# Optimization experiments

Measured on AMD Instinct MI355X. Metric: run time of the kernel, lower is better.

## Reference

```python
import jax, jax.numpy as jnp
import numpy as np

N_NODES = 50000
N_EDGES = 1600000
IN_FEATS = 128
HID = 128
HEADS = 4
F_HEAD = HID // HEADS  # 32
NEG_SLOPE = 0.2


def setup_inputs() -> dict:
    key = jax.random.key(0)
    ks = jax.random.split(key, 7)
    feat = jax.random.normal(ks[0], (N_NODES, IN_FEATS), dtype=jnp.float32)
    # Xavier-ish scaling for the shared fc weight
    W = jax.random.normal(ks[1], (IN_FEATS, HID), dtype=jnp.float32) * (1.0 / np.sqrt(IN_FEATS))
    attn_l = jax.random.normal(ks[2], (HEADS, F_HEAD), dtype=jnp.float32) * 0.1
    attn_r = jax.random.normal(ks[3], (HEADS, F_HEAD), dtype=jnp.float32) * 0.1
    bias = jnp.zeros((HID,), dtype=jnp.float32)
    src_idx = jax.random.randint(ks[4], (N_EDGES,), 0, N_NODES, dtype=jnp.int32)
    dst_idx = jax.random.randint(ks[5], (N_EDGES,), 0, N_NODES, dtype=jnp.int32)
    return {"feat": feat, "W": W, "attn_l": attn_l, "attn_r": attn_r,
            "bias": bias, "src_idx": src_idx, "dst_idx": dst_idx}


def reference(feat, W, attn_l, attn_r, bias, src_idx, dst_idx):
    N = feat.shape[0]
    # shared linear projection, split into heads: [N, H, F]
    ft = (feat @ W).reshape(N, HEADS, F_HEAD)
    # per-node attention logits: [N, H]
    el = jnp.einsum('nhf,hf->nh', ft, attn_l)
    er = jnp.einsum('nhf,hf->nh', ft, attn_r)
    # per-edge unnormalized score: [E, H]
    e = jax.nn.leaky_relu(el[src_idx] + er[dst_idx], negative_slope=NEG_SLOPE)
    # numerically stable edge softmax grouped by destination node
    m = jax.ops.segment_max(e, dst_idx, num_segments=N)          # [N, H]
    m = jnp.where(jnp.isfinite(m), m, 0.0)                       # guard empty dst
    a = jnp.exp(e - m[dst_idx])                                  # [E, H]
    s = jax.ops.segment_sum(a, dst_idx, num_segments=N)          # [N, H]
    alpha = a / jnp.where(s[dst_idx] > 0, s[dst_idx], 1.0)       # [E, H]
    # weighted scatter-sum aggregation: [N, H, F]
    msgs = ft[src_idx] * alpha[:, :, None]
    out = jax.ops.segment_sum(msgs, dst_idx, num_segments=N)
    out = out + bias.reshape(1, HEADS, F_HEAD)
    return out.reshape(N, HEADS * F_HEAD)  # flatten(1)
```

## Files before the change

### kernel.cpp

```cpp
#include <hip/hip_runtime.h>
#include <hip/hip_bf16.h>
#include <math.h>

#define NEG_SLOPE 0.2f
#define NBMAX 1024
#define CAP_E 2560
#define CH 4096

typedef __attribute__((ext_vector_type(8))) short short8;
typedef __attribute__((ext_vector_type(4))) float f32x4;
union BU { uint4 u; short8 s; };

__device__ __forceinline__ unsigned bf16rne(float f) {
    unsigned u = __float_as_uint(f);
    return (u + 0x7fffu + ((u >> 16) & 1u)) >> 16;
}
__device__ __forceinline__ short bf16s(float f) { return (short)bf16rne(f); }

__global__ __launch_bounds__(1024) void k_prepscat(
    const float* __restrict__ W, const float* __restrict__ attn_l,
    const float* __restrict__ attn_r, uint4* __restrict__ Wfrag,
    float4* __restrict__ WL, float4* __restrict__ WR,
    const int* __restrict__ src, const int* __restrict__ dst,
    int* __restrict__ gcur, unsigned* __restrict__ B, int E, int NB) {
    if (blockIdx.x < 3) {
        int gtid = blockIdx.x * 1024 + threadIdx.x;
        if (gtid < 2048) {
            int lane = gtid & 63;
            int ki = (gtid >> 6) & 3;
            int t = (gtid >> 8) & 3;
            int cg = gtid >> 10;
            int col = cg * 64 + t * 16 + (lane & 15);
            int kb = ki * 32 + (lane >> 4) * 8;
            unsigned d[4];
#pragma unroll
            for (int p = 0; p < 4; ++p) {
                unsigned lo = bf16rne(W[(kb + 2 * p) * 128 + col]);
                unsigned hi = bf16rne(W[(kb + 2 * p + 1) * 128 + col]);
                d[p] = lo | (hi << 16);
            }
            Wfrag[gtid] = make_uint4(d[0], d[1], d[2], d[3]);
        } else if (gtid < 2048 + 128) {
            int k = gtid - 2048;
            const float* wr_ = W + k * 128;
            float l0 = 0, l1 = 0, l2 = 0, l3 = 0, r0 = 0, r1 = 0, r2 = 0, r3 = 0;
            for (int j = 0; j < 32; ++j) {
                l0 += wr_[j] * attn_l[j];
                l1 += wr_[32 + j] * attn_l[32 + j];
                l2 += wr_[64 + j] * attn_l[64 + j];
                l3 += wr_[96 + j] * attn_l[96 + j];
                r0 += wr_[j] * attn_r[j];
                r1 += wr_[32 + j] * attn_r[32 + j];
                r2 += wr_[64 + j] * attn_r[64 + j];
                r3 += wr_[96 + j] * attn_r[96 + j];
            }
            WL[k] = make_float4(l0, l1, l2, l3);
            WR[k] = make_float4(r0, r1, r2, r3);
        }
        return;
    }
    __shared__ int h[NBMAX];
    __shared__ int lc[NBMAX];
    __shared__ int dl[CH];
    int tid = threadIdx.x;
    for (int t = tid; t < NB; t += 1024) h[t] = 0;
    __syncthreads();
    int beg = (blockIdx.x - 3) * CH;
    int end = min(beg + CH, E);
    for (int i = beg + tid; i < end; i += 1024) {
        int d = dst[i];
        dl[i - beg] = d;
        atomicAdd(&h[d >> 6], 1);
    }
    __syncthreads();
    for (int t = tid; t < NB; t += 1024)
        lc[t] = (h[t] > 0) ? atomicAdd(&gcur[t], h[t]) : 0;
    __syncthreads();
    for (int i = beg + tid; i < end; i += 1024) {
        int d = dl[i - beg];
        int pos = atomicAdd(&lc[d >> 6], 1);
        if (pos < CAP_E)
            B[(size_t)(d >> 6) * CAP_E + pos] = ((unsigned)src[i] << 6) | (unsigned)(d & 63);
    }
}

__global__ __launch_bounds__(512) void k_fcsort(
    const unsigned* __restrict__ B, const int* __restrict__ gcur,
    unsigned short* __restrict__ srt16, uint2* __restrict__ od,
    const float* __restrict__ feat, const uint4* __restrict__ Wfrag,
    const f32x4* __restrict__ WL, const f32x4* __restrict__ WR,
    unsigned* __restrict__ ftbf, float* __restrict__ el, float* __restrict__ er,
    int N, int NB) {
    __shared__ f32x4 WLs[128], WRs[128];
    __shared__ int hist[64];
    __shared__ int cur[64];
    const int tid = threadIdx.x;

    if (blockIdx.x < NB) {
        const int b = blockIdx.x;
        const int m = min(gcur[b], CAP_E);
        const size_t base = (size_t)b * CAP_E;
        if (tid < 64) hist[tid] = 0;
        __syncthreads();
        for (int i = tid; i < m; i += 512) atomicAdd(&hist[B[base + i] & 63], 1);
        __syncthreads();
        int v0 = (tid < 64) ? hist[tid] : 0;
        for (int off = 1; off < 64; off <<= 1) {
            int t = (tid < 64 && tid >= off) ? hist[tid - off] : 0;
            __syncthreads();
            if (tid < 64) hist[tid] += t;
            __syncthreads();
        }
        if (tid < 64) {
            int ex = hist[tid] - v0;
            cur[tid] = ex;
            int node = (b << 6) + tid;
            if (node < N) od[node] = make_uint2((unsigned)(base + ex), (unsigned)v0);
        }
        __syncthreads();
        for (int i = tid; i < m; i += 512) {
            unsigned p = B[base + i];
            int pos = atomicAdd(&cur[p & 63], 1);
            srt16[base + pos] = (unsigned short)(p >> 6);
        }
        return;
    }

    const int fb = blockIdx.x - NB;
    if (tid < 128) WLs[tid] = WL[tid];
    else if (tid < 256) WRs[tid - 128] = WR[tid - 128];
    __syncthreads();
    const int sub = tid >> 8;
    const int t256 = tid & 255;
    const int wave4 = t256 >> 6;
    const int lane = tid & 63;
    const int rt = wave4 & 1, cg = wave4 >> 1;
    const int nbase = fb * 64 + sub * 32 + rt * 16;
    const int row = nbase + (lane & 15);
    const int rowc = min(row, N - 1);
    const int q = lane >> 4;

    BU b[4][4];
#pragma unroll
    for (int t = 0; t < 4; ++t)
#pragma unroll
        for (int ki = 0; ki < 4; ++ki)
            b[t][ki].u = Wfrag[cg * 1024 + t * 256 + ki * 64 + lane];

    f32x4 acc0 = {0, 0, 0, 0}, acc1 = {0, 0, 0, 0}, acc2 = {0, 0, 0, 0}, acc3 = {0, 0, 0, 0};
    f32x4 elacc = {0, 0, 0, 0}, eracc = {0, 0, 0, 0};
    const float* fr = feat + (size_t)rowc * 128;
#pragma unroll
    for (int ki = 0; ki < 4; ++ki) {
        float4 f0 = *(const float4*)(fr + ki * 32 + q * 8);
        float4 f1 = *(const float4*)(fr + ki * 32 + q * 8 + 4);
        short8 a;
        a[0] = bf16s(f0.x); a[1] = bf16s(f0.y); a[2] = bf16s(f0.z); a[3] = bf16s(f0.w);
        a[4] = bf16s(f1.x); a[5] = bf16s(f1.y); a[6] = bf16s(f1.z); a[7] = bf16s(f1.w);
        acc0 = __builtin_amdgcn_mfma_f32_16x16x32_bf16(a, b[0][ki].s, acc0, 0, 0, 0);
        acc1 = __builtin_amdgcn_mfma_f32_16x16x32_bf16(a, b[1][ki].s, acc1, 0, 0, 0);
        acc2 = __builtin_amdgcn_mfma_f32_16x16x32_bf16(a, b[2][ki].s, acc2, 0, 0, 0);
        acc3 = __builtin_amdgcn_mfma_f32_16x16x32_bf16(a, b[3][ki].s, acc3, 0, 0, 0);
        if (cg == 0) {
            int kb = ki * 32 + q * 8;
            elacc += f0.x * WLs[kb + 0]; eracc += f0.x * WRs[kb + 0];
            elacc += f0.y * WLs[kb + 1]; eracc += f0.y * WRs[kb + 1];
            elacc += f0.z * WLs[kb + 2]; eracc += f0.z * WRs[kb + 2];
            elacc += f0.w * WLs[kb + 3]; eracc += f0.w * WRs[kb + 3];
            elacc += f1.x * WLs[kb + 4]; eracc += f1.x * WRs[kb + 4];
            elacc += f1.y * WLs[kb + 5]; eracc += f1.y * WRs[kb + 5];
            elacc += f1.z * WLs[kb + 6]; eracc += f1.z * WRs[kb + 6];
            elacc += f1.w * WLs[kb + 7]; eracc += f1.w * WRs[kb + 7];
        }
    }
#pragma unroll
    for (int t = 0; t < 4; ++t) {
#pragma unroll
        for (int r = 0; r < 4; ++r) {
            float d = (t == 0) ? acc0[r] : (t == 1) ? acc1[r] : (t == 2) ? acc2[r] : acc3[r];
            unsigned m = bf16rne(d);
            unsigned nb = (unsigned)__shfl_xor((int)m, 1, 64);
            int node = nbase + q * 4 + r;
            if (!(lane & 1) && node < N)
                ftbf[(size_t)node * 64 + cg * 32 + t * 8 + ((lane & 15) >> 1)] = m | (nb << 16);
        }
    }
    if (cg == 0) {
#pragma unroll
        for (int c = 0; c < 4; ++c) {
            elacc[c] += __shfl_xor(elacc[c], 16, 64);
            eracc[c] += __shfl_xor(eracc[c], 16, 64);
            elacc[c] += __shfl_xor(elacc[c], 32, 64);
            eracc[c] += __shfl_xor(eracc[c], 32, 64);
        }
        if (lane < 16 && row < N) {
            *(float4*)(el + (size_t)row * 4) = make_float4(elacc[0], elacc[1], elacc[2], elacc[3]);
            *(float4*)(er + (size_t)row * 4) = make_float4(eracc[0], eracc[1], eracc[2], eracc[3]);
        }
    }
}

__global__ __launch_bounds__(256) void k_aggregate(
    const unsigned* __restrict__ ftbf, const float* __restrict__ el,
    const float* __restrict__ er, const unsigned short* __restrict__ srt16,
    const uint2* __restrict__ od, const float* __restrict__ bias,
    float* __restrict__ out, int N) {
    __shared__ float als[4][64][4];
    __shared__ int snl[4][64];
    const int wave = threadIdx.x >> 6;
    const int lane = threadIdx.x & 63;
    const int l15 = lane & 15;
    const int hd = l15 >> 2;
    const int g = lane >> 4;
    int node = blockIdx.x * 4 + wave;
    if (node >= N) return;
    uint2 o = od[node];
    int beg = (int)o.x, cnt = (int)o.y;
    float4 erd = *(const float4*)(er + (size_t)node * 4);
    const uint4* ftv = (const uint4*)ftbf;

    float s0 = 0.f, s1 = 0.f, s2 = 0.f, s3 = 0.f;
    float ac0 = 0, ac1 = 0, ac2 = 0, ac3 = 0, ac4 = 0, ac5 = 0, ac6 = 0, ac7 = 0;
    for (int tile = 0; tile < cnt; tile += 64) {
        int tc = min(64, cnt - tile);
        float a0 = 0.f, a1 = 0.f, a2 = 0.f, a3 = 0.f;
        int sn = 0;
        if (lane < tc) {
            sn = srt16[beg + tile + lane];
            float4 a = *(const float4*)(el + (size_t)sn * 4);
            float e0 = a.x + erd.x; e0 = fmaxf(e0, NEG_SLOPE * e0);
            float e1 = a.y + erd.y; e1 = fmaxf(e1, NEG_SLOPE * e1);
            float e2 = a.z + erd.z; e2 = fmaxf(e2, NEG_SLOPE * e2);
            float e3 = a.w + erd.w; e3 = fmaxf(e3, NEG_SLOPE * e3);
            a0 = __expf(e0); a1 = __expf(e1);
            a2 = __expf(e2); a3 = __expf(e3);
        }
        s0 += a0; s1 += a1; s2 += a2; s3 += a3;
        *(float4*)(&als[wave][lane][0]) = make_float4(a0, a1, a2, a3);
        snl[wave][lane] = sn;
#pragma unroll 2
        for (int jj0 = 0; jj0 < tc; jj0 += 4) {
            int jj = jj0 + g;
            int j2 = (jj < tc) ? jj : (tc - 1);
            float af = als[wave][j2][hd];
            if (jj >= tc) af = 0.f;
            int s = snl[wave][j2];
            uint4 u = ftv[((size_t)s << 4) + l15];
            ac0 = fmaf(__uint_as_float(u.x << 16), af, ac0);
            ac1 = fmaf(__uint_as_float(u.x & 0xffff0000u), af, ac1);
            ac2 = fmaf(__uint_as_float(u.y << 16), af, ac2);
            ac3 = fmaf(__uint_as_float(u.y & 0xffff0000u), af, ac3);
            ac4 = fmaf(__uint_as_float(u.z << 16), af, ac4);
            ac5 = fmaf(__uint_as_float(u.z & 0xffff0000u), af, ac5);
            ac6 = fmaf(__uint_as_float(u.w << 16), af, ac6);
            ac7 = fmaf(__uint_as_float(u.w & 0xffff0000u), af, ac7);
        }
    }
#pragma unroll
    for (int off = 16; off <= 32; off <<= 1) {
        ac0 += __shfl_xor(ac0, off, 64);
        ac1 += __shfl_xor(ac1, off, 64);
        ac2 += __shfl_xor(ac2, off, 64);
        ac3 += __shfl_xor(ac3, off, 64);
        ac4 += __shfl_xor(ac4, off, 64);
        ac5 += __shfl_xor(ac5, off, 64);
        ac6 += __shfl_xor(ac6, off, 64);
        ac7 += __shfl_xor(ac7, off, 64);
    }
#pragma unroll
    for (int off = 32; off >= 1; off >>= 1) {
        s0 += __shfl_xor(s0, off, 64);
        s1 += __shfl_xor(s1, off, 64);
        s2 += __shfl_xor(s2, off, 64);
        s3 += __shfl_xor(s3, off, 64);
    }
    float ssel = (hd == 0) ? s0 : (hd == 1) ? s1 : (hd == 2) ? s2 : s3;
    float inv = ssel > 0.f ? 1.f / ssel : 0.f;
    if (lane < 16) {
        int c0 = lane * 8;
        float4 b0 = *(const float4*)(bias + c0);
        float4 b1 = *(const float4*)(bias + c0 + 4);
        float4 o0, o1;
        o0.x = ac0 * inv + b0.x; o0.y = ac1 * inv + b0.y;
        o0.z = ac2 * inv + b0.z; o0.w = ac3 * inv + b0.w;
        o1.x = ac4 * inv + b1.x; o1.y = ac5 * inv + b1.y;
        o1.z = ac6 * inv + b1.z; o1.w = ac7 * inv + b1.w;
        *(float4*)(out + (size_t)node * 128 + c0) = o0;
        *(float4*)(out + (size_t)node * 128 + c0 + 4) = o1;
    }
}

extern "C" void kernel_launch(void* const* d_in, const int* in_sizes, int n_in,
                              void* d_out, int out_size, void* d_ws, size_t ws_size,
                              hipStream_t stream) {
    const float* feat = (const float*)d_in[0];
    const float* W = (const float*)d_in[1];
    const float* attn_l = (const float*)d_in[2];
    const float* attn_r = (const float*)d_in[3];
    const float* bias = (const float*)d_in[4];
    const int* src = (const int*)d_in[5];
    const int* dst = (const int*)d_in[6];
    const int N = in_sizes[0] / 128;
    const int E = in_sizes[5];
    const int NB = (N + 63) >> 6;
    float* out = (float*)d_out;

    char* p = (char*)d_ws;
    unsigned int* ftbf = (unsigned int*)p;      p += (size_t)N * 64 * 4;
    unsigned* B = (unsigned*)p;                 p += ((size_t)NB * CAP_E * 4 + 15) & ~15ull;
    unsigned short* srt16 = (unsigned short*)p; p += ((size_t)NB * CAP_E * 2 + 15) & ~15ull;
    float* el = (float*)p;                      p += (size_t)N * 4 * 4;
    float* er = (float*)p;                      p += (size_t)N * 4 * 4;
    uint2* od = (uint2*)p;                      p += (size_t)N * 8;
    int* gcur = (int*)p;                        p += ((size_t)NB * 4 + 15) & ~15ull;
    uint4* Wfrag = (uint4*)p;                   p += 2048 * 16;
    float4* WL = (float4*)p;                    p += 128 * 16;
    float4* WR = (float4*)p;                    p += 128 * 16;

    int eblocks = (E + CH - 1) / CH;
    int fcblocks = (N + 63) / 64;
    hipMemsetAsync(gcur, 0, (size_t)NB * 4, stream);
    k_prepscat<<<3 + eblocks, 1024, 0, stream>>>(W, attn_l, attn_r, Wfrag, WL, WR,
                                                 src, dst, gcur, B, E, NB);
    k_fcsort<<<NB + fcblocks, 512, 0, stream>>>(B, gcur, srt16, od, feat, Wfrag,
                                                (const f32x4*)WL, (const f32x4*)WR,
                                                ftbf, el, er, N, NB);
    k_aggregate<<<(N + 3) / 4, 256, 0, stream>>>(ftbf, el, er, srt16, od, bias, out, N);
}
```

Baseline: 111.9 us.

## Regroup kernels so edge scatter overlaps node projection, split sort out

```diff
diff --git a/kernel.cpp b/kernel.cpp
--- a/kernel.cpp
+++ b/kernel.cpp
@@ -5,7 +5,7 @@
 #define NEG_SLOPE 0.2f
 #define NBMAX 1024
 #define CAP_E 2560
-#define CH 4096
+#define CH 8192
 
 typedef __attribute__((ext_vector_type(8))) short short8;
 typedef __attribute__((ext_vector_type(4))) float f32x4;
@@ -17,116 +17,84 @@
 }
 __device__ __forceinline__ short bf16s(float f) { return (short)bf16rne(f); }
 
-__global__ __launch_bounds__(1024) void k_prepscat(
+__global__ __launch_bounds__(1024) void k_prep0(
     const float* __restrict__ W, const float* __restrict__ attn_l,
     const float* __restrict__ attn_r, uint4* __restrict__ Wfrag,
     float4* __restrict__ WL, float4* __restrict__ WR,
+    int* __restrict__ gcur, int NB) {
+    int gtid = blockIdx.x * 1024 + threadIdx.x;
+    if (gtid < 2048) {
+        int lane = gtid & 63;
+        int ki = (gtid >> 6) & 3;
+        int t = (gtid >> 8) & 3;
+        int cg = gtid >> 10;
+        int col = cg * 64 + t * 16 + (lane & 15);
+        int kb = ki * 32 + (lane >> 4) * 8;
+        unsigned d[4];
+#pragma unroll
+        for (int p = 0; p < 4; ++p) {
+            unsigned lo = bf16rne(W[(kb + 2 * p) * 128 + col]);
+            unsigned hi = bf16rne(W[(kb + 2 * p + 1) * 128 + col]);
+            d[p] = lo | (hi << 16);
+        }
+        Wfrag[gtid] = make_uint4(d[0], d[1], d[2], d[3]);
+    } else if (gtid < 2048 + 128) {
+        int k = gtid - 2048;
+        const float* wr_ = W + k * 128;
+        float l0 = 0, l1 = 0, l2 = 0, l3 = 0, r0 = 0, r1 = 0, r2 = 0, r3 = 0;
+        for (int j = 0; j < 32; ++j) {
+            l0 += wr_[j] * attn_l[j];
+            l1 += wr_[32 + j] * attn_l[32 + j];
+            l2 += wr_[64 + j] * attn_l[64 + j];
+            l3 += wr_[96 + j] * attn_l[96 + j];
+            r0 += wr_[j] * attn_r[j];
+            r1 += wr_[32 + j] * attn_r[32 + j];
+            r2 += wr_[64 + j] * attn_r[64 + j];
+            r3 += wr_[96 + j] * attn_r[96 + j];
+        }
+        WL[k] = make_float4(l0, l1, l2, l3);
+        WR[k] = make_float4(r0, r1, r2, r3);
+    } else if (gtid - 2176 < NB) {
+        gcur[gtid - 2176] = 0;
+    }
+}
+
+__global__ __launch_bounds__(512) void k_megascat(
     const int* __restrict__ src, const int* __restrict__ dst,
-    int* __restrict__ gcur, unsigned* __restrict__ B, int E, int NB) {
-    if (blockIdx.x < 3) {
-        int gtid = blockIdx.x * 1024 + threadIdx.x;
-        if (gtid < 2048) {
-            int lane = gtid & 63;
-            int ki = (gtid >> 6) & 3;
-            int t = (gtid >> 8) & 3;
-            int cg = gtid >> 10;
-            int col = cg * 64 + t * 16 + (lane & 15);
-            int kb = ki * 32 + (lane >> 4) * 8;
-            unsigned d[4];
-#pragma unroll
-            for (int p = 0; p < 4; ++p) {
-                unsigned lo = bf16rne(W[(kb + 2 * p) * 128 + col]);
-                unsigned hi = bf16rne(W[(kb + 2 * p + 1) * 128 + col]);
-                d[p] = lo | (hi << 16);
-            }
-            Wfrag[gtid] = make_uint4(d[0], d[1], d[2], d[3]);
-        } else if (gtid < 2048 + 128) {
-            int k = gtid - 2048;
-            const float* wr_ = W + k * 128;
-            float l0 = 0, l1 = 0, l2 = 0, l3 = 0, r0 = 0, r1 = 0, r2 = 0, r3 = 0;
-            for (int j = 0; j < 32; ++j) {
-                l0 += wr_[j] * attn_l[j];
-                l1 += wr_[32 + j] * attn_l[32 + j];
-                l2 += wr_[64 + j] * attn_l[64 + j];
-                l3 += wr_[96 + j] * attn_l[96 + j];
-                r0 += wr_[j] * attn_r[j];
-                r1 += wr_[32 + j] * attn_r[32 + j];
-                r2 += wr_[64 + j] * attn_r[64 + j];
-                r3 += wr_[96 + j] * attn_r[96 + j];
-            }
-            WL[k] = make_float4(l0, l1, l2, l3);
-            WR[k] = make_float4(r0, r1, r2, r3);
-        }
-        return;
-    }
-    __shared__ int h[NBMAX];
-    __shared__ int lc[NBMAX];
-    __shared__ int dl[CH];
-    int tid = threadIdx.x;
-    for (int t = tid; t < NB; t += 1024) h[t] = 0;
-    __syncthreads();
-    int beg = (blockIdx.x - 3) * CH;
-    int end = min(beg + CH, E);
-    for (int i = beg + tid; i < end; i += 1024) {
-        int d = dst[i];
-        dl[i - beg] = d;
-        atomicAdd(&h[d >> 6], 1);
-    }
-    __syncthreads();
-    for (int t = tid; t < NB; t += 1024)
-        lc[t] = (h[t] > 0) ? atomicAdd(&gcur[t], h[t]) : 0;
-    __syncthreads();
-    for (int i = beg + tid; i < end; i += 1024) {
-        int d = dl[i - beg];
-        int pos = atomicAdd(&lc[d >> 6], 1);
-        if (pos < CAP_E)
-            B[(size_t)(d >> 6) * CAP_E + pos] = ((unsigned)src[i] << 6) | (unsigned)(d & 63);
-    }
-}
-
-__global__ __launch_bounds__(512) void k_fcsort(
-    const unsigned* __restrict__ B, const int* __restrict__ gcur,
-    unsigned short* __restrict__ srt16, uint2* __restrict__ od,
+    int* __restrict__ gcur, unsigned* __restrict__ B, int E, int SB,
     const float* __restrict__ feat, const uint4* __restrict__ Wfrag,
     const f32x4* __restrict__ WL, const f32x4* __restrict__ WR,
     unsigned* __restrict__ ftbf, float* __restrict__ el, float* __restrict__ er,
     int N, int NB) {
+    const int tid = threadIdx.x;
+    if (blockIdx.x < SB) {
+        __shared__ int h[NBMAX];
+        __shared__ int lc[NBMAX];
+        __shared__ int dl[CH];
+        for (int t = tid; t < NB; t += 512) h[t] = 0;
+        __syncthreads();
+        int beg = blockIdx.x * CH;
+        int end = min(beg + CH, E);
+        for (int i = beg + tid; i < end; i += 512) {
+            int d = dst[i];
+            dl[i - beg] = d;
+            atomicAdd(&h[d >> 6], 1);
+        }
+        __syncthreads();
+        for (int t = tid; t < NB; t += 512)
+            lc[t] = (h[t] > 0) ? atomicAdd(&gcur[t], h[t]) : 0;
+        __syncthreads();
+        for (int i = beg + tid; i < end; i += 512) {
+            int d = dl[i - beg];
+            int pos = atomicAdd(&lc[d >> 6], 1);
+            if (pos < CAP_E)
+                B[(size_t)(d >> 6) * CAP_E + pos] = ((unsigned)src[i] << 6) | (unsigned)(d & 63);
+        }
+        return;
+    }
+
     __shared__ f32x4 WLs[128], WRs[128];
-    __shared__ int hist[64];
-    __shared__ int cur[64];
-    const int tid = threadIdx.x;
-
-    if (blockIdx.x < NB) {
-        const int b = blockIdx.x;
-        const int m = min(gcur[b], CAP_E);
-        const size_t base = (size_t)b * CAP_E;
-        if (tid < 64) hist[tid] = 0;
-        __syncthreads();
-        for (int i = tid; i < m; i += 512) atomicAdd(&hist[B[base + i] & 63], 1);
-        __syncthreads();
-        int v0 = (tid < 64) ? hist[tid] : 0;
-        for (int off = 1; off < 64; off <<= 1) {
-            int t = (tid < 64 && tid >= off) ? hist[tid - off] : 0;
-            __syncthreads();
-            if (tid < 64) hist[tid] += t;
-            __syncthreads();
-        }
-        if (tid < 64) {
-            int ex = hist[tid] - v0;
-            cur[tid] = ex;
-            int node = (b << 6) + tid;
-            if (node < N) od[node] = make_uint2((unsigned)(base + ex), (unsigned)v0);
-        }
-        __syncthreads();
-        for (int i = tid; i < m; i += 512) {
-            unsigned p = B[base + i];
-            int pos = atomicAdd(&cur[p & 63], 1);
-            srt16[base + pos] = (unsigned short)(p >> 6);
-        }
-        return;
-    }
-
-    const int fb = blockIdx.x - NB;
+    const int fb = blockIdx.x - SB;
     if (tid < 128) WLs[tid] = WL[tid];
     else if (tid < 256) WRs[tid - 128] = WR[tid - 128];
     __syncthreads();
@@ -200,6 +168,40 @@
     }
 }
 
+__global__ __launch_bounds__(512) void k_sort(
+    const unsigned* __restrict__ B, const int* __restrict__ gcur,
+    unsigned short* __restrict__ srt16, uint2* __restrict__ od, int N) {
+    __shared__ int hist[64];
+    __shared__ int cur[64];
+    const int tid = threadIdx.x;
+    const int b = blockIdx.x;
+    const int m = min(gcur[b], CAP_E);
+    const size_t base = (size_t)b * CAP_E;
+    if (tid < 64) hist[tid] = 0;
+    __syncthreads();
+    for (int i = tid; i < m; i += 512) atomicAdd(&hist[B[base + i] & 63], 1);
+    __syncthreads();
+    int v0 = (tid < 64) ? hist[tid] : 0;
+    for (int off = 1; off < 64; off <<= 1) {
+        int t = (tid < 64 && tid >= off) ? hist[tid - off] : 0;
+        __syncthreads();
+        if (tid < 64) hist[tid] += t;
+        __syncthreads();
+    }
+    if (tid < 64) {
+        int ex = hist[tid] - v0;
+        cur[tid] = ex;
+        int node = (b << 6) + tid;
+        if (node < N) od[node] = make_uint2((unsigned)(base + ex), (unsigned)v0);
+    }
+    __syncthreads();
+    for (int i = tid; i < m; i += 512) {
+        unsigned p = B[base + i];
+        int pos = atomicAdd(&cur[p & 63], 1);
+        srt16[base + pos] = (unsigned short)(p >> 6);
+    }
+}
+
 __global__ __launch_bounds__(256) void k_aggregate(
     const unsigned* __restrict__ ftbf, const float* __restrict__ el,
     const float* __restrict__ er, const unsigned short* __restrict__ srt16,
@@ -319,11 +321,11 @@
 
     int eblocks = (E + CH - 1) / CH;
     int fcblocks = (N + 63) / 64;
-    hipMemsetAsync(gcur, 0, (size_t)NB * 4, stream);
-    k_prepscat<<<3 + eblocks, 1024, 0, stream>>>(W, attn_l, attn_r, Wfrag, WL, WR,
-                                                 src, dst, gcur, B, E, NB);
-    k_fcsort<<<NB + fcblocks, 512, 0, stream>>>(B, gcur, srt16, od, feat, Wfrag,
-                                                (const f32x4*)WL, (const f32x4*)WR,
-                                                ftbf, el, er, N, NB);
+    k_prep0<<<4, 1024, 0, stream>>>(W, attn_l, attn_r, Wfrag, WL, WR, gcur, NB);
+    k_megascat<<<eblocks + fcblocks, 512, 0, stream>>>(src, dst, gcur, B, E, eblocks,
+                                                       feat, Wfrag, (const f32x4*)WL,
+                                                       (const f32x4*)WR, ftbf, el, er,
+                                                       N, NB);
+    k_sort<<<NB, 512, 0, stream>>>(B, gcur, srt16, od, N);
     k_aggregate<<<(N + 3) / 4, 256, 0, stream>>>(ftbf, el, er, srt16, od, bias, out, N);
 }
```

New measurement: 110.5 us. About the same (-1.3%).
